# Kernel tuning notes

Hardware: AMD Instinct MI355X
Metric: run time of the kernel (lower is better)

The kernel has to match this reference:

```python
import math
import jax, jax.numpy as jnp
import numpy as np
from jax import lax

B, S, T = 16, 1200, 600
D, V, FF = 1024, 1404, 2048
H, DH, PERIOD, WID = 4, 256, 25, 8


def setup_inputs() -> dict:
    key = jax.random.key(0)
    ks = jax.random.split(key, 24)
    w = lambda i, shape: jax.random.normal(ks[i], shape, dtype=jnp.float32) * 0.02
    return {
        "audio_embedding": jax.random.normal(ks[0], (B, S, 768), dtype=jnp.float32),
        "vertice": jax.random.normal(ks[1], (B, T, 3, 468), dtype=jnp.float32),
        "W_af": w(2, (D, 768)), "b_af": w(3, (D,)),
        "sa_Wq": w(4, (D, D)), "sa_bq": w(5, (D,)),
        "sa_Wk": w(6, (D, D)), "sa_bk": w(7, (D,)),
        "sa_Wv": w(8, (D, D)), "sa_bv": w(9, (D,)),
        "sa_Wo": w(10, (D, D)), "sa_bo": w(11, (D,)),
        "ca_Wq": w(12, (D, D)), "ca_bq": w(13, (D,)),
        "ca_Wk": w(14, (D, D)), "ca_bk": w(15, (D,)),
        "ca_Wv": w(16, (D, D)), "ca_bv": w(17, (D,)),
        "ca_Wo": w(18, (D, D)), "ca_bo": w(19, (D,)),
        "ln1_g": jnp.ones((D,), jnp.float32), "ln1_b": jnp.zeros((D,), jnp.float32),
        "ln2_g": jnp.ones((D,), jnp.float32), "ln2_b": jnp.zeros((D,), jnp.float32),
        "ln3_g": jnp.ones((D,), jnp.float32), "ln3_b": jnp.zeros((D,), jnp.float32),
        "W_ff1": w(20, (FF, D)), "b_ff1": jnp.zeros((FF,), jnp.float32),
        "W_ff2": w(21, (D, FF)), "b_ff2": jnp.zeros((D,), jnp.float32),
        "W_vm": w(22, (D, V)), "b_vm": jnp.zeros((D,), jnp.float32),
        "W_vr": w(23, (V, D)), "b_vr": jnp.zeros((V,), jnp.float32),
    }


def _pe_table():
    # PeriodicPositionalEncoding: sin/cos table of length `period`, tiled over time
    pos = np.arange(PERIOD, dtype=np.float32)[:, None]
    div = np.exp(np.arange(0, D, 2, dtype=np.float32) * (-math.log(10000.0) / D))
    pe = np.zeros((PERIOD, D), dtype=np.float32)
    pe[:, 0::2] = np.sin(pos * div)
    pe[:, 1::2] = np.cos(pos * div)
    return jnp.asarray(pe)


def _slopes():
    start = 2.0 ** (-2.0 ** (-(math.log2(H) - 3.0)))
    return jnp.asarray(start * start ** np.arange(H, dtype=np.float32), dtype=jnp.float32)


def _ln(x, g, b):
    m = jnp.mean(x, -1, keepdims=True)
    v = jnp.mean((x - m) ** 2, -1, keepdims=True)
    return (x - m) / jnp.sqrt(v + 1e-5) * g + b


def reference(audio_embedding, vertice, W_af, b_af, sa_Wq, sa_bq, sa_Wk, sa_bk, sa_Wv, sa_bv, sa_Wo, sa_bo, ca_Wq, ca_bq, ca_Wk, ca_bk, ca_Wv, ca_bv, ca_Wo, ca_bo, ln1_g, ln1_b, ln2_g, ln2_b, ln3_g, ln3_b, W_ff1, b_ff1, W_ff2, b_ff2, W_vm, b_vm, W_vr, b_vr):
    # The torch loop reruns the full causal decoder on the growing prefix each frame;
    # because the tgt mask is strictly causal (ALiBi bias depends only on i-j), the
    # math is exactly equivalent to an incremental decode with a self-attn KV cache.
    pe, slopes = _pe_table(), _slopes()
    scale = 1.0 / math.sqrt(DH)
    NEG = -1e9
    hidden = audio_embedding @ W_af.T + b_af              # (B,S,D) audio_feature_map
    mem_k = (hidden @ ca_Wk.T + ca_bk).reshape(B, S, H, DH)
    mem_v = (hidden @ ca_Wv.T + ca_bv).reshape(B, S, H, DH)
    t_idx = jnp.arange(T)
    s_idx = jnp.arange(S)
    emb0 = jnp.broadcast_to(b_vm, (B, D))                 # vertice_map(zeros)
    kc0 = jnp.zeros((T, B, D), jnp.float32)
    vc0 = jnp.zeros((T, B, D), jnp.float32)

    def step(carry, i):
        emb, kc, vc = carry
        x = emb + pe[i % PERIOD]                          # PPE (B,D)
        q = (x @ sa_Wq.T + sa_bq).reshape(B, H, DH)
        kc = kc.at[i].set(x @ sa_Wk.T + sa_bk)
        vc = vc.at[i].set(x @ sa_Wv.T + sa_bv)
        kh = kc.reshape(T, B, H, DH)
        vh = vc.reshape(T, B, H, DH)
        rel = i - t_idx                                   # ALiBi: alibi[i,j] = -floor((i-j)/period)
        bias = slopes[:, None] * (-(jnp.maximum(rel, 0) // PERIOD)).astype(jnp.float32)
        sc = jnp.einsum('bhd,tbhd->bht', q, kh) * scale + bias[None]
        sc = jnp.where((t_idx <= i)[None, None, :], sc, NEG)
        sa = jnp.einsum('bht,tbhd->bhd', jax.nn.softmax(sc, -1), vh).reshape(B, D)
        x = _ln(x + sa @ sa_Wo.T + sa_bo, ln1_g, ln1_b)
        q2 = (x @ ca_Wq.T + ca_bq).reshape(B, H, DH)
        sc2 = jnp.einsum('bhd,bshd->bhs', q2, mem_k) * scale
        allowed = (s_idx >= 2 * i - (WID - 2)) & (s_idx < 2 * i + 2)   # enc_dec_mask window
        sc2 = jnp.where(allowed[None, None, :], sc2, NEG)
        ca = jnp.einsum('bhs,bshd->bhd', jax.nn.softmax(sc2, -1), mem_v).reshape(B, D)
        x = _ln(x + ca @ ca_Wo.T + ca_bo, ln2_g, ln2_b)
        ff = jax.nn.relu(x @ W_ff1.T + b_ff1) @ W_ff2.T + b_ff2
        x = _ln(x + ff, ln3_g, ln3_b)
        out_v = x @ W_vr.T + b_vr                         # vertice_map_r (B,V)
        emb_next = out_v @ W_vm.T + b_vm                  # vertice_map of last output
        return (emb_next, kc, vc), out_v

    _, outs = lax.scan(step, (emb0, kc0, vc0), t_idx)
    vertice_out = jnp.transpose(outs, (1, 0, 2))          # (B,T,V)
    loss = jnp.mean((vertice_out - vertice.reshape(B, T, -1)) ** 2)
    return loss
```

## Files before the change

### kernel.cpp

```cpp
#include <hip/hip_runtime.h>

typedef unsigned short u16;
typedef short s16x8 __attribute__((ext_vector_type(8)));
typedef float f32x4 __attribute__((ext_vector_type(4)));
typedef float f32x2 __attribute__((ext_vector_type(2)));
typedef unsigned u32x2 __attribute__((ext_vector_type(2)));

#define DEV static __device__ __forceinline__

DEV float bf2f(u16 h){ union{unsigned u;float f;} v; v.u=((unsigned)h)<<16; return v.f; }
DEV u16 f2bf(float f){ union{float f;unsigned u;} v; v.f=f; unsigned u=v.u; return (u16)((u + 0x7fffu + ((u>>16)&1u))>>16); }

DEV void st2_dc(u16* p, u16 v){
  unsigned vv = v;
  asm volatile("global_store_short %0, %1, off sc0 sc1" :: "v"(p), "v"(vv) : "memory");
}
DEV void st16_dc(void* p, s16x8 v){
  asm volatile("global_store_dwordx4 %0, %1, off sc0 sc1" :: "v"(p), "v"(v) : "memory");
}
DEV void stf_dc(float* p, float v){
  asm volatile("global_store_dword %0, %1, off sc0 sc1" :: "v"(p), "v"(v) : "memory");
}
DEV u16 ld2_dc(const u16* p){
  unsigned r;
  asm volatile("global_load_ushort %0, %1, off sc0 sc1\n\ts_waitcnt vmcnt(0)" : "=&v"(r) : "v"(p) : "memory");
  return (u16)r;
}
DEV u32x2 ld8_dc2(const u16* p){
  u32x2 r;
  asm volatile("global_load_dwordx2 %0, %1, off sc0 sc1\n\ts_waitcnt vmcnt(0)" : "=&v"(r) : "v"(p) : "memory");
  return r;
}
DEV void vmwait0(){ asm volatile("s_waitcnt vmcnt(0)" ::: "memory"); }

DEV void ldf8_dc(const u16* p, s16x8* o){
  asm volatile(
    "global_load_dwordx4 %0, %8, off sc0 sc1\n\t"
    "global_load_dwordx4 %1, %8, off offset:64 sc0 sc1\n\t"
    "global_load_dwordx4 %2, %8, off offset:128 sc0 sc1\n\t"
    "global_load_dwordx4 %3, %8, off offset:192 sc0 sc1\n\t"
    "global_load_dwordx4 %4, %8, off offset:256 sc0 sc1\n\t"
    "global_load_dwordx4 %5, %8, off offset:320 sc0 sc1\n\t"
    "global_load_dwordx4 %6, %8, off offset:384 sc0 sc1\n\t"
    "global_load_dwordx4 %7, %8, off offset:448 sc0 sc1\n\t"
    "s_waitcnt vmcnt(0)"
    : "=&v"(o[0]),"=&v"(o[1]),"=&v"(o[2]),"=&v"(o[3]),
      "=&v"(o[4]),"=&v"(o[5]),"=&v"(o[6]),"=&v"(o[7])
    : "v"(p) : "memory");
}
DEV void ldf8r_dc(const u16* p, s16x8* o, const u16* pr, unsigned* rr){
  asm volatile(
    "global_load_dwordx4 %0, %9, off sc0 sc1\n\t"
    "global_load_dwordx4 %1, %9, off offset:64 sc0 sc1\n\t"
    "global_load_dwordx4 %2, %9, off offset:128 sc0 sc1\n\t"
    "global_load_dwordx4 %3, %9, off offset:192 sc0 sc1\n\t"
    "global_load_dwordx4 %4, %9, off offset:256 sc0 sc1\n\t"
    "global_load_dwordx4 %5, %9, off offset:320 sc0 sc1\n\t"
    "global_load_dwordx4 %6, %9, off offset:384 sc0 sc1\n\t"
    "global_load_dwordx4 %7, %9, off offset:448 sc0 sc1\n\t"
    "global_load_ushort %8, %10, off sc0 sc1\n\t"
    "s_waitcnt vmcnt(0)"
    : "=&v"(o[0]),"=&v"(o[1]),"=&v"(o[2]),"=&v"(o[3]),
      "=&v"(o[4]),"=&v"(o[5]),"=&v"(o[6]),"=&v"(o[7]),"=&v"(*rr)
    : "v"(p), "v"(pr) : "memory");
}
DEV void ldf8rs_dc(const u16* p, s16x8* o, const u16* pr, unsigned* rr, const float* ps, f32x2* ss){
  asm volatile(
    "global_load_dwordx4 %0, %10, off sc0 sc1\n\t"
    "global_load_dwordx4 %1, %10, off offset:64 sc0 sc1\n\t"
    "global_load_dwordx4 %2, %10, off offset:128 sc0 sc1\n\t"
    "global_load_dwordx4 %3, %10, off offset:192 sc0 sc1\n\t"
    "global_load_dwordx4 %4, %10, off offset:256 sc0 sc1\n\t"
    "global_load_dwordx4 %5, %10, off offset:320 sc0 sc1\n\t"
    "global_load_dwordx4 %6, %10, off offset:384 sc0 sc1\n\t"
    "global_load_dwordx4 %7, %10, off offset:448 sc0 sc1\n\t"
    "global_load_ushort %8, %11, off sc0 sc1\n\t"
    "global_load_dwordx2 %9, %12, off sc0 sc1\n\t"
    "s_waitcnt vmcnt(0)"
    : "=&v"(o[0]),"=&v"(o[1]),"=&v"(o[2]),"=&v"(o[3]),
      "=&v"(o[4]),"=&v"(o[5]),"=&v"(o[6]),"=&v"(o[7]),"=&v"(*rr),"=&v"(*ss)
    : "v"(p), "v"(pr), "v"(ps) : "memory");
}
DEV void ldf16rs_dc(const u16* p, s16x8* o, const u16* pr, unsigned* rr, const float* ps, f32x2* ss){
  asm volatile(
    "global_load_dwordx4 %0, %18, off sc0 sc1\n\t"
    "global_load_dwordx4 %1, %18, off offset:64 sc0 sc1\n\t"
    "global_load_dwordx4 %2, %18, off offset:128 sc0 sc1\n\t"
    "global_load_dwordx4 %3, %18, off offset:192 sc0 sc1\n\t"
    "global_load_dwordx4 %4, %18, off offset:256 sc0 sc1\n\t"
    "global_load_dwordx4 %5, %18, off offset:320 sc0 sc1\n\t"
    "global_load_dwordx4 %6, %18, off offset:384 sc0 sc1\n\t"
    "global_load_dwordx4 %7, %18, off offset:448 sc0 sc1\n\t"
    "global_load_dwordx4 %8, %18, off offset:2048 sc0 sc1\n\t"
    "global_load_dwordx4 %9, %18, off offset:2112 sc0 sc1\n\t"
    "global_load_dwordx4 %10, %18, off offset:2176 sc0 sc1\n\t"
    "global_load_dwordx4 %11, %18, off offset:2240 sc0 sc1\n\t"
    "global_load_dwordx4 %12, %18, off offset:2304 sc0 sc1\n\t"
    "global_load_dwordx4 %13, %18, off offset:2368 sc0 sc1\n\t"
    "global_load_dwordx4 %14, %18, off offset:2432 sc0 sc1\n\t"
    "global_load_dwordx4 %15, %18, off offset:2496 sc0 sc1\n\t"
    "global_load_ushort %16, %19, off sc0 sc1\n\t"
    "global_load_dwordx2 %17, %20, off sc0 sc1\n\t"
    "s_waitcnt vmcnt(0)"
    : "=&v"(o[0]),"=&v"(o[1]),"=&v"(o[2]),"=&v"(o[3]),
      "=&v"(o[4]),"=&v"(o[5]),"=&v"(o[6]),"=&v"(o[7]),
      "=&v"(o[8]),"=&v"(o[9]),"=&v"(o[10]),"=&v"(o[11]),
      "=&v"(o[12]),"=&v"(o[13]),"=&v"(o[14]),"=&v"(o[15]),
      "=&v"(*rr),"=&v"(*ss)
    : "v"(p), "v"(pr), "v"(ps) : "memory");
}

constexpr size_t SZ_DD = (size_t)1024*1024*2;
constexpr size_t OFF_WQ2=0;
constexpr size_t OFF_WK2=OFF_WQ2+SZ_DD;
constexpr size_t OFF_WV2=OFF_WK2+SZ_DD;
constexpr size_t OFF_WO=OFF_WV2+SZ_DD;
constexpr size_t OFF_CAWQ=OFF_WO+SZ_DD;
constexpr size_t OFF_CAWO=OFF_CAWQ+SZ_DD;
constexpr size_t OFF_FF1=OFF_CAWO+SZ_DD;
constexpr size_t OFF_FF2=OFF_FF1+(size_t)2048*1024*2;
constexpr size_t OFF_MB =OFF_FF2+(size_t)2048*1024*2;
constexpr size_t OFF_WVR=OFF_MB+SZ_DD;
constexpr size_t OFF_WKP=OFF_WVR+(size_t)1404*1024*2;
constexpr size_t OFF_WVP=OFF_WKP+(size_t)1024*768*2;
constexpr size_t OFF_WAFT=OFF_WVP+(size_t)1024*768*2;
constexpr size_t OFF_WVRT=OFF_WAFT+(size_t)768*1024*2;
constexpr size_t OFF_PE  =OFF_WVRT+(size_t)1024*1408*2;
constexpr size_t OFF_BKP =OFF_PE+25*1024*4;
constexpr size_t OFF_BVP =OFF_BKP+4096;
constexpr size_t OFF_BCOMB=OFF_BVP+4096;
constexpr size_t OFF_MEMK=OFF_BCOMB+4096;
constexpr size_t OFF_MEMV=OFF_MEMK+(size_t)16*1200*1024*2;
constexpr size_t OFF_KC  =OFF_MEMV+(size_t)16*1200*1024*2;
constexpr size_t OFF_VC  =OFF_KC+(size_t)600*16*1024*2;
constexpr size_t OFF_U3S =OFF_VC+(size_t)600*16*1024*2;
constexpr size_t OFF_ST3 =OFF_U3S+(size_t)600*16*1024*2;
constexpr size_t OFF_XB  =OFF_ST3+600*32*4;
constexpr size_t OFF_QB  =OFF_XB+32768;
constexpr size_t OFF_SC  =OFF_QB+32768;
constexpr size_t OFF_SA  =OFF_SC+(size_t)16*4*608*4;
constexpr size_t OFF_U1  =OFF_SA+32768;
constexpr size_t OFF_ST1 =OFF_U1+32768;
constexpr size_t OFF_Q2  =OFF_ST1+256;
constexpr size_t OFF_CA  =OFF_Q2+32768;
constexpr size_t OFF_U2  =OFF_CA+32768;
constexpr size_t OFF_ST2 =OFF_U2+32768;
constexpr size_t OFF_HH  =OFF_ST2+256;
constexpr size_t OFF_LOSS=OFF_HH+65536;
constexpr size_t OFF_BAR =OFF_LOSS+256;
constexpr size_t OFF_MBT =OFF_BAR+32768;
constexpr size_t OFF_AT  =OFF_MBT+SZ_DD;
constexpr size_t WS_NEED =OFF_AT+(size_t)3*25*1024*4;

DEV float gemm_frag(const s16x8* a, const u16* slot, float* FB){
  int tid=threadIdx.x, wv=tid>>6, ln=tid&63;
  int r=ln&15, kq=ln>>4;
  int k0=wv*256 + kq*8;
  int sw=(r&7)<<3;
  const u16* bp = slot + r*1024;
  f32x4 acc={0.f,0.f,0.f,0.f};
  #pragma unroll
  for(int j=0;j<8;j++)
    acc = __builtin_amdgcn_mfma_f32_16x16x32_bf16(a[j], *(const s16x8*)(bp + ((k0+32*j)^sw)), acc, 0,0,0);
  #pragma unroll
  for(int j=0;j<4;j++) FB[wv*256 + (kq*4+j)*16 + r] = acc[j];
  __syncthreads();
  int row=tid>>4, col=tid&15;
  float s=(FB[row*16+col]+FB[256+row*16+col])+(FB[512+row*16+col]+FB[768+row*16+col]);
  __syncthreads();
  return s;
}

DEV void ln_frags(s16x8* a, const float* g, const float* be, int k0, int r, float* RB, float* STm, float* STr){
  int tid=threadIdx.x;
  float sum=0.f, sq=0.f;
  #pragma unroll
  for(int j=0;j<8;j++){
    #pragma unroll
    for(int e=0;e<8;e++){ float f=bf2f((u16)a[j][e]); sum+=f; sq+=f*f; }
  }
  RB[tid]=sum; RB[256+tid]=sq;
  __syncthreads();
  if (tid<16){
    float S=0.f,Q=0.f;
    #pragma unroll
    for(int q=0;q<16;q++){ S+=RB[tid+16*q]; Q+=RB[256+tid+16*q]; }
    float m=S*(1.f/1024.f); float var=Q*(1.f/1024.f)-m*m;
    STm[tid]=m; STr[tid]=rsqrtf(var+1e-5f);
  }
  __syncthreads();
  float m=STm[r], rs=STr[r];
  const float* gg=g+k0; const float* bb=be+k0;
  #pragma unroll
  for(int j=0;j<8;j++){
    s16x8 o;
    #pragma unroll
    for(int e=0;e<8;e++){ int k=32*j+e; float f=(bf2f((u16)a[j][e])-m)*rs*gg[k]+bb[k]; o[e]=(short)f2bf(f); }
    a[j]=o;
  }
}

DEV void copy_slot(const u16* src, int rstride, u16* dst){
  int row=threadIdx.x>>4, k0=(threadIdx.x&15)<<6;
  int sw=(row&7)<<3;
  const u16* s = src + (size_t)row*rstride + k0;
  u16* d = dst + row*1024;
  #pragma unroll
  for(int c=0;c<64;c+=8)
    *(s16x8*)(d + (((k0+c))^sw)) = *(const s16x8*)(s+c);
}

DEV void gbar(char* barb, unsigned& epoch, int wg){
  vmwait0();
  __syncthreads();
  unsigned target = epoch + 1u;
  if (threadIdx.x == 0)
    __hip_atomic_store((unsigned*)(barb + (wg<<7)), target, __ATOMIC_RELAXED, __HIP_MEMORY_SCOPE_AGENT);
  {
    unsigned* s = (unsigned*)(barb + (threadIdx.x<<7));
    while (__hip_atomic_load(s, __ATOMIC_RELAXED, __HIP_MEMORY_SCOPE_AGENT) < target)
      __builtin_amdgcn_s_sleep(1);
  }
  __syncthreads();
  epoch++;
}

__global__ void __launch_bounds__(256) k_init(float* pe, float* loss, unsigned* bar){
  int tid=threadIdx.x;
  if (tid==0) loss[0]=0.f;
  for(int idx=tid; idx<8192; idx+=256) bar[idx]=0u;
  for(int idx=tid; idx<25600; idx+=256){
    int p_=idx>>10, d_=idx&1023; int m=d_>>1;
    float div = expf(-(float)(2*m) * (9.210340372f/1024.f));
    float a = (float)p_ * div;
    pe[idx] = (d_&1)? cosf(a) : sinf(a);
  }
}

__global__ void __launch_bounds__(256) k_f2bf(const float* s, u16* d, int n){
  int idx=(blockIdx.x*256+threadIdx.x)*8;
  if (idx < n){
    #pragma unroll
    for(int j=0;j<8;j++) d[idx+j]=f2bf(s[idx+j]);
  }
}

__global__ void __launch_bounds__(256) k_tr(const float* src, int R, int C, u16* dst, int ldd){
  __shared__ float TL[32][33];
  int cb=(C+31)/32;
  int bj=blockIdx.x%cb, br=blockIdx.x/cb;
  int j0=bj*32, r0=br*32;
  int lj=threadIdx.x&31, lr=threadIdx.x>>5;
  #pragma unroll
  for(int p=0;p<4;p++){ int rr=r0+lr+p*8, jj=j0+lj;
    TL[lr+p*8][lj] = (rr<R && jj<C)? src[(size_t)rr*C+jj] : 0.f; }
  __syncthreads();
  #pragma unroll
  for(int p=0;p<4;p++){ int jj=j0+lr+p*8, rr=r0+lj;
    if (jj<C && rr<ldd) dst[(size_t)jj*ldd+rr] = f2bf(TL[lj][lr+p*8]); }
}

__global__ void __launch_bounds__(256) k_trb(const u16* src, u16* dst){
  __shared__ u16 T[32][33];
  int bi=blockIdx.x>>5, bj=blockIdx.x&31;
  int li=threadIdx.x>>5, lj=threadIdx.x&31;
  #pragma unroll
  for(int p=0;p<4;p++) T[li+p*8][lj] = src[(size_t)(bi*32+li+p*8)*1024 + bj*32+lj];
  __syncthreads();
  #pragma unroll
  for(int p=0;p<4;p++) dst[(size_t)(bj*32+li+p*8)*1024 + bi*32+lj] = T[lj][li+p*8];
}

DEV float gemm_tile16g(const u16* SLu, int lds_stride, const u16* W, int Kext, int wstride, int colbase, float* FB){
  int tid=threadIdx.x, wv=tid>>6, ln=tid&63;
  int r=ln&15, kq=ln>>4;
  int kpw=Kext>>2, k0=wv*kpw;
  const u16* ap = SLu + r*lds_stride + k0 + kq*8;
  const u16* bp = W + (size_t)(colbase+r)*wstride + k0 + kq*8;
  f32x4 acc={0.f,0.f,0.f,0.f};
  for(int k=0;k<kpw;k+=32)
    acc = __builtin_amdgcn_mfma_f32_16x16x32_bf16(*(const s16x8*)(ap+k), *(const s16x8*)(bp+k), acc, 0,0,0);
  #pragma unroll
  for(int j=0;j<4;j++) FB[wv*256 + (kq*4+j)*16 + r] = acc[j];
  __syncthreads();
  int row=tid>>4, col=tid&15;
  float s=(FB[row*16+col]+FB[256+row*16+col])+(FB[512+row*16+col]+FB[768+row*16+col]);
  __syncthreads();
  return s;
}

__global__ void __launch_bounds__(256) k_gemm_pre(const float* A, int lda, int Kreal, int Kpad,
                                                  const u16* Bw, u16* out, int ldo, int Ntiles){
  __shared__ u16 SL[16*1416];
  __shared__ float FB[1024];
  int bx=blockIdx.x; int mt=bx/Ntiles, nt=bx%Ntiles;
  int tid=threadIdx.x;
  int cpt = Kpad>>4;
  { int row=tid>>4, c0=(tid&15)*cpt;
    const float* s=A + (size_t)(mt*16+row)*lda;
    u16* d=SL + row*(Kpad+8);
    for(int c=0;c<cpt;c++){ int k=c0+c; d[k] = (k<Kreal)? f2bf(s[k]) : (u16)0; }
    __syncthreads();
  }
  float v = gemm_tile16g(SL, Kpad+8, Bw, Kpad, Kpad, nt*16, FB);
  int row=tid>>4, col=tid&15;
  out[(size_t)(mt*16+row)*ldo + nt*16+col] = f2bf(v);
}

__global__ void __launch_bounds__(256) k_bvec(const float* caWk, const float* ca_bk, const float* b_af,
                                              const float* caWv, const float* ca_bv,
                                              const float* Wvm, const float* b_vr, const float* b_vm,
                                              float* bkp, float* bvp, float* bcomb){
  __shared__ float VB[1408];
  int seg=blockIdx.x>>2, ch=blockIdx.x&3; int o=ch*256+threadIdx.x;
  const float* vec = (seg==2)? b_vr : b_af; int K = (seg==2)?1404:1024;
  for(int k=threadIdx.x;k<K;k+=256) VB[k]=vec[k];
  __syncthreads();
  const float* Arow = (seg==0)? caWk+(size_t)o*1024 : (seg==1)? caWv+(size_t)o*1024 : Wvm+(size_t)o*1404;
  float s=0.f;
  for(int k=0;k<K;k++) s += Arow[k]*VB[k];
  if(seg==0) bkp[o]=s+ca_bk[o]; else if(seg==1) bvp[o]=s+ca_bv[o]; else bcomb[o]=s+b_vm[o];
}

__global__ void __launch_bounds__(256) k_afold(const float* pe, const float* bcomb,
                                               const float* Wq, const float* Wk, const float* Wv,
                                               const float* bq, const float* bk, const float* bv,
                                               float* at){
  __shared__ float XV[1024];
  int bx=blockIdx.x; int mat=bx/100; int rem=bx%100; int ip=rem>>2; int ch=rem&3;
  const float* W = (mat==0)?Wq:(mat==1)?Wk:Wv;
  const float* bias = (mat==0)?bq:(mat==1)?bk:bv;
  for(int o=threadIdx.x;o<1024;o+=256) XV[o]=bcomb[o]+pe[ip*1024+o];
  __syncthreads();
  int c = ch*256+threadIdx.x;
  const float* wr = W + (size_t)c*1024;
  float acc=0.f;
  for(int o=0;o<1024;o++) acc += XV[o]*wr[o];
  at[((size_t)mat*25+ip)*1024+c] = acc + bias[c];
}

__global__ void __launch_bounds__(256) k_qkv0(const float* b_vm, const float* pe,
                                              const float* Wq, const float* Wk, const float* Wv,
                                              const float* bq, const float* bk, const float* bv,
                                              u16* qb, u16* kc, u16* vc, u16* xb){
  __shared__ float XV[1024];
  int bx=blockIdx.x; int mat=bx&3, ch=bx>>2;
  for(int o=threadIdx.x;o<1024;o+=256) XV[o]=b_vm[o]+pe[o];
  __syncthreads();
  int c = ch*256+threadIdx.x;
  if (mat==3){
    u16 hv = f2bf(XV[c]);
    for(int r=0;r<16;r++) xb[r*1024+c]=hv;
  } else {
    const float* W = (mat==0)?Wq:(mat==1)?Wk:Wv;
    const float* bias = (mat==0)?bq:(mat==1)?bk:bv;
    const float* wr = W + (size_t)c*1024;
    float acc=0.f;
    for(int o=0;o<1024;o++) acc += XV[o]*wr[o];
    u16 hv = f2bf(acc + bias[c]);
    u16* dst = (mat==0)? qb : (mat==1)? kc : vc;
    for(int r=0;r<16;r++) dst[r*1024+c]=hv;
  }
}

__global__ void __launch_bounds__(256) k_mem(const float* audio, const u16* wkp, const u16* wvp,
                                             const float* bkp, const float* bvp, u16* mt8, u16* memv){
  __shared__ u16 SL[16*776];
  int bx=blockIdx.x; int mt=bx>>3, cbk=bx&7;
  int tid=threadIdx.x, wv=tid>>6, ln=tid&63;
  { int row=tid>>4, c0=(tid&15)*48;
    const float* s = audio + (size_t)(mt*16+row)*768 + c0;
    u16* d = SL + row*776 + c0;
    #pragma unroll
    for(int c=0;c<48;c+=8){ s16x8 o;
      #pragma unroll
      for(int j=0;j<8;j++) o[j]=(short)f2bf(s[c+j]);
      *(s16x8*)(d+c)=o; }
    __syncthreads();
  }
  int r=ln&15, kq=ln>>4;
  const u16* ap = SL + r*776 + kq*8;
  for(int rep=0;rep<2;rep++){
    int colb = cbk*128 + wv*32 + rep*16;
    for(int mat=0;mat<2;mat++){
      const u16* W = mat? wvp : wkp;
      const u16* bp = W + (size_t)(colb+r)*768 + kq*8;
      f32x4 acc={0.f,0.f,0.f,0.f};
      for(int k=0;k<768;k+=32)
        acc = __builtin_amdgcn_mfma_f32_16x16x32_bf16(*(const s16x8*)(ap+k), *(const s16x8*)(bp+k), acc, 0,0,0);
      const float* bias = mat? bvp:bkp;
      int o = colb + r;
      float bo = bias[o];
      #pragma unroll
      for(int j=0;j<4;j++){ int row_=kq*4+j;
        int g = mt*16+row_;
        float val = acc[j] + bo;
        if (mat){
          memv[(size_t)g*1024 + o] = f2bf(val);
        } else {
          int bb=g/1200, ss=g-bb*1200;
          mt8[(((size_t)(bb*4 + (o>>8))*32 + ((o&255)>>3))*1200 + ss)*8 + (o&7)] = f2bf(val);
        }
      }
    }
  }
}

struct LoopArgs {
  const float *sa_bo,*ca_bq,*ca_bo,*b_ff1,*b_ff2;
  const float *g1,*be1,*g2,*be2,*g3,*be3;
  char* ws;
};

__global__ void __launch_bounds__(256,1) k_loop(LoopArgs A){
  __shared__ u16 WL[3*16*1024];
  __shared__ float FB[1024];
  __shared__ float PL[608];
  __shared__ float RB[640];
  __shared__ float STm[16], STr[16];

  char* ws = A.ws;
  const u16* wq2  =(const u16*)(ws+OFF_WQ2);
  const u16* wk2  =(const u16*)(ws+OFF_WK2);
  const u16* wv2  =(const u16*)(ws+OFF_WV2);
  const u16* wo   =(const u16*)(ws+OFF_WO);
  const u16* cawq =(const u16*)(ws+OFF_CAWQ);
  const u16* cawo =(const u16*)(ws+OFF_CAWO);
  const u16* ff1  =(const u16*)(ws+OFF_FF1);
  const u16* ff2  =(const u16*)(ws+OFF_FF2);
  const u16* mb   =(const u16*)(ws+OFF_MB);
  const float* pe =(const float*)(ws+OFF_PE);
  const float* bcomb=(const float*)(ws+OFF_BCOMB);
  const float* at =(const float*)(ws+OFF_AT);
  const u16* mt8  =(const u16*)(ws+OFF_MEMK);
  const u16* memv =(const u16*)(ws+OFF_MEMV);
  u16* kc =(u16*)(ws+OFF_KC);
  u16* vc =(u16*)(ws+OFF_VC);
  u16* u3s=(u16*)(ws+OFF_U3S);
  float* st3=(float*)(ws+OFF_ST3);
  u16* xb =(u16*)(ws+OFF_XB);
  u16* qb =(u16*)(ws+OFF_QB);
  u16* sab=(u16*)(ws+OFF_SA);
  u16* u1 =(u16*)(ws+OFF_U1);
  float* st1=(float*)(ws+OFF_ST1);
  u16* cab=(u16*)(ws+OFF_CA);
  u16* u2 =(u16*)(ws+OFF_U2);
  float* st2=(float*)(ws+OFF_ST2);
  u16* hh =(u16*)(ws+OFF_HH);
  char* barb=(char*)(ws+OFF_BAR);

  unsigned epoch = 0;
  int wg = blockIdx.x, tid = threadIdx.x;
  int row = tid>>4, lo = tid&15;
  int wv = tid>>6, ln = tid&63;
  int fr = ln&15, kq = ln>>4;
  int k0 = wv*256 + kq*8;
  int grp = wg>>6, ct = (wg&63)<<4;

  {
    u16* s0d = WL;          u16* s1d = WL+16384;  u16* s2d = WL+32768;
    if (grp==0){
      copy_slot(wq2 +(size_t)ct*1024,1024,s0d);
      copy_slot(ff1 +(size_t)ct*1024,1024,s2d);
    } else if (grp==1){
      copy_slot(wk2 +(size_t)ct*1024,1024,s0d);
      copy_slot(cawo+(size_t)ct*1024,1024,s1d);
      copy_slot(ff1 +((size_t)(1024+ct))*1024,1024,s2d);
    } else if (grp==2){
      copy_slot(wv2 +(size_t)ct*1024,1024,s0d);
      copy_slot(ff2 +(size_t)ct*2048,2048,s1d);
      copy_slot(ff2 +(size_t)ct*2048+1024,2048,s2d);
    } else {
      copy_slot(mb  +(size_t)ct*1024,1024,s0d);
      copy_slot(wo  +(size_t)ct*1024,1024,s1d);
    }
    __syncthreads();
  }
  const u16* SLOT0 = WL;
  const u16* SLOT1 = WL+16384;
  const u16* SLOT2 = WL+32768;

  #pragma unroll 1
  for (int i=0;i<600;i++){

    if (wg < 64){
      int b=wg>>2, h=wg&3, cnt=i+1;
      RB[tid] = bf2f(ld2_dc(qb + b*1024 + h*256 + tid));
      __syncthreads();
      float sl = 1.0f/(float)(4<<(2*h));
      float mloc=-1e30f, lloc=0.f;
      for(int t=tid; t<cnt; t+=256){
        const u16* kr = kc + ((size_t)t*16 + b)*1024 + h*256;
        float s=0.f;
        #pragma unroll
        for(int c=0;c<256;c+=8){
          s16x8 k8 = *(const s16x8*)(kr+c);
          #pragma unroll
          for(int j=0;j<8;j++) s += RB[c+j]*bf2f((u16)k8[j]);
        }
        s = s*0.0625f - sl*(float)((i-t)/25);
        PL[t]=s;
        float M = fmaxf(mloc, s);
        lloc = lloc*__expf(mloc-M) + __expf(s-M);
        mloc = M;
      }
      #pragma unroll
      for(int off=32; off>0; off>>=1){
        float m2=__shfl_xor(mloc,off), l2=__shfl_xor(lloc,off);
        float M=fmaxf(mloc,m2);
        lloc = lloc*__expf(mloc-M) + l2*__expf(m2-M);
        mloc = M;
      }
      if (ln==0){ RB[576+2*wv]=mloc; RB[577+2*wv]=lloc; }
      __syncthreads();
      float M=-1e30f, L=0.f;
      #pragma unroll
      for(int w=0;w<4;w++){
        float m2=RB[576+2*w], l2=RB[577+2*w];
        float Mn=fmaxf(M,m2);
        L = L*__expf(M-Mn) + l2*__expf(m2-Mn);
        M = Mn;
      }
      float rl = 1.0f/L;
      int d_oct = tid>>3, t_ln = tid&7;
      const u16* vcb = vc + (size_t)b*1024 + h*256 + d_oct*8;
      float acc[8]={0.f,0.f,0.f,0.f,0.f,0.f,0.f,0.f};
      for(int t=t_ln; t<cnt; t+=8){
        s16x8 v8 = *(const s16x8*)(vcb + (size_t)t*16384);
        float p = __expf(PL[t]-M);
        #pragma unroll
        for(int jj=0;jj<8;jj++) acc[jj] += p*bf2f((u16)v8[jj]);
      }
      #pragma unroll
      for(int j=0;j<8;j++){
        acc[j] += __shfl_xor(acc[j],1);
        acc[j] += __shfl_xor(acc[j],2);
        acc[j] += __shfl_xor(acc[j],4);
      }
      if (t_ln==0){
        s16x8 o8;
        #pragma unroll
        for(int j=0;j<8;j++) o8[j]=(short)f2bf(acc[j]*rl);
        st16_dc(sab + b*1024 + h*256 + d_oct*8, o8);
      }
    }
    gbar(barb, epoch, wg);

    if (wg>=192){
      s16x8 f[8]; unsigned er;
      ldf8r_dc(sab + fr*1024 + k0, f, xb + row*1024 + ct + lo, &er);
      float v = gemm_frag(f,SLOT1,FB);
      int o = ct+lo;
      st2_dc(u1 + row*1024 + o, f2bf(bf2f((u16)er) + v + A.sa_bo[o]));
    }
    gbar(barb, epoch, wg);

    if (wg<64){
      int b=wg>>2, h=wg&3;
      u32x2 uu = ld8_dc2(u1 + b*1024 + tid*4);
      float e0=bf2f((u16)(uu[0]&0xffffu)), e1=bf2f((u16)(uu[0]>>16));
      float e2=bf2f((u16)(uu[1]&0xffffu)), e3=bf2f((u16)(uu[1]>>16));
      float s=(e0+e1)+(e2+e3);
      float q=(e0*e0+e1*e1)+(e2*e2+e3*e3);
      #pragma unroll
      for(int o2=32;o2>0;o2>>=1){ s+=__shfl_down(s,o2); q+=__shfl_down(q,o2); }
      if (ln==0){ RB[608+wv]=s; RB[616+wv]=q; }
      __syncthreads();
      float S=(RB[608]+RB[609])+(RB[610]+RB[611]);
      float Q=(RB[616]+RB[617])+(RB[618]+RB[619]);
      float m=S*(1.f/1024.f);
      float rs=rsqrtf(Q*(1.f/1024.f)-m*m+1e-5f);
      if (h==0 && tid==0){ stf_dc(st1+b*2, m); stf_dc(st1+b*2+1, rs); }
      { int k=tid*4;
        FB[k]  =(e0-m)*rs*A.g1[k]  +A.be1[k];
        FB[k+1]=(e1-m)*rs*A.g1[k+1]+A.be1[k+1];
        FB[k+2]=(e2-m)*rs*A.g1[k+2]+A.be1[k+2];
        FB[k+3]=(e3-m)*rs*A.g1[k+3]+A.be1[k+3]; }
      __syncthreads();
      int c = h*256 + tid;
      const u16* wr = cawq + (size_t)c*1024;
      float acc=0.f;
      #pragma unroll 4
      for(int kk=0;kk<128;kk++){
        s16x8 w8 = *(const s16x8*)(wr + kk*8);
        #pragma unroll
        for(int j=0;j<8;j++) acc += FB[kk*8+j]*bf2f((u16)w8[j]);
      }
      RB[tid] = acc + A.ca_bq[c];
      __syncthreads();
      int s0 = 2*i-6; if(s0<0)s0=0;
      int s1 = 2*i+2; if(s1>1200)s1=1200;
      int ns = s1-s0;
      int si=tid>>5, dl=tid&31;
      float p=0.f;
      if (si<ns){
        const u16* MT = mt8 + (((size_t)(b*4+h)*32 + dl)*1200 + (s0+si))*8;
        s16x8 m8 = *(const s16x8*)MT;
        #pragma unroll
        for(int j=0;j<8;j++) p += RB[dl*8+j]*bf2f((u16)m8[j]);
      }
      #pragma unroll
      for(int o2=16;o2>0;o2>>=1) p += __shfl_xor(p,o2);
      if (dl==0 && si<ns) RB[512+si] = p*0.0625f;
      __syncthreads();
      float mx=-1e30f;
      for(int qd=0;qd<ns;qd++) mx=fmaxf(mx,RB[512+qd]);
      float l=0.f, acc2=0.f;
      for(int qd=0;qd<ns;qd++){
        float e=__expf(RB[512+qd]-mx); l+=e;
        acc2 += e*bf2f(memv[(size_t)(b*1200+s0+qd)*1024 + h*256 + tid]);
      }
      st2_dc(cab + b*1024+h*256+tid, f2bf(acc2/l));
    }
    gbar(barb, epoch, wg);

    if (wg>=64 && wg<128){
      s16x8 f[8]; unsigned ur; f32x2 sv;
      ldf8rs_dc(cab + fr*1024 + k0, f, u1 + row*1024 + ct + lo, &ur, st1 + row*2, &sv);
      float v = gemm_frag(f,SLOT1,FB);
      int o=ct+lo;
      float x1 = (bf2f((u16)ur)-sv[0])*sv[1]*A.g1[o] + A.be1[o];
      st2_dc(u2+row*1024+o, f2bf(x1 + v + A.ca_bo[o]));
    }
    gbar(barb, epoch, wg);

    if (wg<128){
      s16x8 f[8];
      ldf8_dc(u2 + fr*1024 + k0, f);
      ln_frags(f, A.g2, A.be2, k0, fr, RB, STm, STr);
      float v = gemm_frag(f,SLOT2,FB);
      int o=(wg<<4)+lo;
      st2_dc(hh+row*2048+o, f2bf(fmaxf(v + A.b_ff1[o], 0.f)));
      if (wg==0 && tid<16){ stf_dc(st2+tid*2,STm[tid]); stf_dc(st2+tid*2+1,STr[tid]); }
    }
    gbar(barb, epoch, wg);

    if (wg>=128 && wg<192){
      s16x8 f[16]; unsigned ur; f32x2 sv;
      ldf16rs_dc(hh + fr*2048 + k0, f, u2 + row*1024 + ct + lo, &ur, st2 + row*2, &sv);
      float v = gemm_frag(f,SLOT1,FB);
      v += gemm_frag(f+8,SLOT2,FB);
      int o=ct+lo;
      float x2 = (bf2f((u16)ur)-sv[0])*sv[1]*A.g2[o] + A.be2[o];
      st2_dc(u3s + ((size_t)i*16+row)*1024+o, f2bf(x2 + v + A.b_ff2[o]));
    }
    gbar(barb, epoch, wg);

    {
      int ipn = (i+1)%25;
      s16x8 f[8];
      ldf8_dc(u3s + (size_t)i*16384 + fr*1024 + k0, f);
      ln_frags(f, A.g3, A.be3, k0, fr, RB, STm, STr);
      float v = gemm_frag(f,SLOT0,FB);
      int o = ct+lo;
      if (grp==0){
        st2_dc(qb + row*1024 + o, f2bf(v + at[(size_t)0*25600 + ipn*1024 + o]));
      } else if (grp==1){
        if (i<599) st2_dc(kc + ((size_t)(i+1)*16+row)*1024 + o, f2bf(v + at[(size_t)1*25600 + ipn*1024 + o]));
      } else if (grp==2){
        if (i<599) st2_dc(vc + ((size_t)(i+1)*16+row)*1024 + o, f2bf(v + at[(size_t)2*25600 + ipn*1024 + o]));
      } else {
        st2_dc(xb + row*1024 + o, f2bf(v + bcomb[o] + pe[ipn*1024+o]));
        if (wg==192 && tid<16){ st3[i*32+tid*2]=STm[tid]; st3[i*32+tid*2+1]=STr[tid]; }
      }
    }
    gbar(barb, epoch, wg);
  }
}

__global__ void __launch_bounds__(256) k_loss(const u16* u3s, const float* st3, const u16* wvr,
                                              const float* bvr, const float* g3, const float* be3,
                                              const float* vert, float* loss){
  __shared__ u16 SL[16*1032];
  __shared__ float R[64];
  int bx=blockIdx.x; int ib=bx/11, cb=bx%11;
  int tid=threadIdx.x, wvv=tid>>6, ln=tid&63;
  int r=ln&15, kq=ln>>4;
  float lsum=0.f;
  for(int ii=0;ii<8;ii++){
    int i=ib*8+ii;
    { int row=tid>>4, c0=(tid&15)<<6;
      float m=st3[i*32+row*2], rs=st3[i*32+row*2+1];
      const u16* s=u3s + (size_t)(i*16+row)*1024 + c0;
      u16* d=SL + row*1032 + c0;
      #pragma unroll
      for(int c=0;c<64;c+=8){ s16x8 v=*(const s16x8*)(s+c); s16x8 o;
        #pragma unroll
        for(int j=0;j<8;j++){ int cc=c0+c+j; o[j]=(short)f2bf((bf2f((u16)v[j])-m)*rs*g3[cc]+be3[cc]); }
        *(s16x8*)(d+c)=o; }
      __syncthreads();
    }
    const u16* ap = SL + r*1032 + kq*8;
    for(int rep=0;rep<2;rep++){
      int colb = cb*128 + wvv*32 + rep*16;
      int o_r = colb + r; bool ok = o_r < 1404;
      const u16* bp = wvr + (size_t)(ok? o_r:0)*1024 + kq*8;
      f32x4 acc={0.f,0.f,0.f,0.f};
      for(int k=0;k<1024;k+=32)
        acc = __builtin_amdgcn_mfma_f32_16x16x32_bf16(*(const s16x8*)(ap+k), *(const s16x8*)(bp+k), acc, 0,0,0);
      if (ok){
        float bo = bvr[o_r];
        #pragma unroll
        for(int j=0;j<4;j++){
          int b_=kq*4+j;
          float ov = acc[j] + bo;
          float vt = vert[(size_t)(b_*600 + i)*1404 + o_r];
          float dd = ov - vt; lsum += dd*dd;
        }
      }
    }
    __syncthreads();
  }
  #pragma unroll
  for(int o=32;o>0;o>>=1) lsum += __shfl_down(lsum,o);
  if (ln==0) R[wvv]=lsum;
  __syncthreads();
  if (tid==0) atomicAdd(loss, (R[0]+R[1])+(R[2]+R[3]));
}

__global__ void k_fin(const float* loss, float* dout){
  if (threadIdx.x==0) dout[0] = loss[0] * (1.f/13478400.f);
}

extern "C" void kernel_launch(void* const* d_in, const int* in_sizes, int n_in,
                              void* d_out, int out_size, void* d_ws, size_t ws_size,
                              hipStream_t stream){
  char* ws = (char*)d_ws;
  if (ws_size < WS_NEED){ hipMemsetAsync(d_out, 0, 4, stream); return; }

  const float* audio=(const float*)d_in[0];
  const float* vert =(const float*)d_in[1];
  const float* W_af =(const float*)d_in[2];
  const float* b_af =(const float*)d_in[3];
  const float* saWq =(const float*)d_in[4];  const float* sa_bq=(const float*)d_in[5];
  const float* saWk =(const float*)d_in[6];  const float* sa_bk=(const float*)d_in[7];
  const float* saWv =(const float*)d_in[8];  const float* sa_bv=(const float*)d_in[9];
  const float* saWo =(const float*)d_in[10]; const float* sa_bo=(const float*)d_in[11];
  const float* caWq =(const float*)d_in[12]; const float* ca_bq=(const float*)d_in[13];
  const float* caWk =(const float*)d_in[14]; const float* ca_bk=(const float*)d_in[15];
  const float* caWv =(const float*)d_in[16]; const float* ca_bv=(const float*)d_in[17];
  const float* caWo =(const float*)d_in[18]; const float* ca_bo=(const float*)d_in[19];
  const float* g1=(const float*)d_in[20]; const float* be1=(const float*)d_in[21];
  const float* g2=(const float*)d_in[22]; const float* be2=(const float*)d_in[23];
  const float* g3=(const float*)d_in[24]; const float* be3=(const float*)d_in[25];
  const float* Wff1=(const float*)d_in[26]; const float* b_ff1=(const float*)d_in[27];
  const float* Wff2=(const float*)d_in[28]; const float* b_ff2=(const float*)d_in[29];
  const float* Wvm=(const float*)d_in[30];  const float* b_vm=(const float*)d_in[31];
  const float* Wvr=(const float*)d_in[32];  const float* b_vr=(const float*)d_in[33];

  k_init<<<1,256,0,stream>>>((float*)(ws+OFF_PE), (float*)(ws+OFF_LOSS), (unsigned*)(ws+OFF_BAR));

  k_f2bf<<<512,256,0,stream>>>(caWq,(u16*)(ws+OFF_CAWQ),1048576);
  k_f2bf<<<512,256,0,stream>>>(caWo,(u16*)(ws+OFF_CAWO),1048576);
  k_f2bf<<<512,256,0,stream>>>(saWo,(u16*)(ws+OFF_WO),1048576);
  k_f2bf<<<1024,256,0,stream>>>(Wff1,(u16*)(ws+OFF_FF1),2097152);
  k_f2bf<<<1024,256,0,stream>>>(Wff2,(u16*)(ws+OFF_FF2),2097152);
  k_f2bf<<<702,256,0,stream>>>(Wvr,(u16*)(ws+OFF_WVR),1437696);

  k_tr<<<24*32,256,0,stream>>>(W_af, 1024, 768, (u16*)(ws+OFF_WAFT), 1024);
  k_tr<<<32*44,256,0,stream>>>(Wvr, 1404, 1024, (u16*)(ws+OFF_WVRT), 1408);

  k_gemm_pre<<<64*48,256,0,stream>>>(caWk, 1024, 1024, 1024, (const u16*)(ws+OFF_WAFT), (u16*)(ws+OFF_WKP), 768, 48);
  k_gemm_pre<<<64*48,256,0,stream>>>(caWv, 1024, 1024, 1024, (const u16*)(ws+OFF_WAFT), (u16*)(ws+OFF_WVP), 768, 48);
  k_gemm_pre<<<64*64,256,0,stream>>>(Wvm, 1404, 1404, 1408, (const u16*)(ws+OFF_WVRT), (u16*)(ws+OFF_MB), 1024, 64);

  k_trb<<<1024,256,0,stream>>>((const u16*)(ws+OFF_MB), (u16*)(ws+OFF_MBT));
  k_gemm_pre<<<64*64,256,0,stream>>>(saWq, 1024, 1024, 1024, (const u16*)(ws+OFF_MBT), (u16*)(ws+OFF_WQ2), 1024, 64);
  k_gemm_pre<<<64*64,256,0,stream>>>(saWk, 1024, 1024, 1024, (const u16*)(ws+OFF_MBT), (u16*)(ws+OFF_WK2), 1024, 64);
  k_gemm_pre<<<64*64,256,0,stream>>>(saWv, 1024, 1024, 1024, (const u16*)(ws+OFF_MBT), (u16*)(ws+OFF_WV2), 1024, 64);

  k_bvec<<<12,256,0,stream>>>(caWk, ca_bk, b_af, caWv, ca_bv, Wvm, b_vr, b_vm,
                              (float*)(ws+OFF_BKP),(float*)(ws+OFF_BVP),(float*)(ws+OFF_BCOMB));

  k_afold<<<300,256,0,stream>>>((const float*)(ws+OFF_PE), (const float*)(ws+OFF_BCOMB),
                                saWq, saWk, saWv, sa_bq, sa_bk, sa_bv, (float*)(ws+OFF_AT));

  k_qkv0<<<16,256,0,stream>>>(b_vm, (const float*)(ws+OFF_PE), saWq, saWk, saWv, sa_bq, sa_bk, sa_bv,
                              (u16*)(ws+OFF_QB), (u16*)(ws+OFF_KC), (u16*)(ws+OFF_VC), (u16*)(ws+OFF_XB));

  k_mem<<<9600,256,0,stream>>>(audio, (const u16*)(ws+OFF_WKP),(const u16*)(ws+OFF_WVP),
                               (const float*)(ws+OFF_BKP),(const float*)(ws+OFF_BVP),
                               (u16*)(ws+OFF_MEMK),(u16*)(ws+OFF_MEMV));

  LoopArgs la{ sa_bo, ca_bq, ca_bo, b_ff1, b_ff2,
               g1, be1, g2, be2, g3, be3, ws };
  k_loop<<<256,256,0,stream>>>(la);

  k_loss<<<825,256,0,stream>>>((const u16*)(ws+OFF_U3S),(const float*)(ws+OFF_ST3),
                               (const u16*)(ws+OFF_WVR), b_vr, g3, be3, vert, (float*)(ws+OFF_LOSS));
  k_fin<<<1,64,0,stream>>>((const float*)(ws+OFF_LOSS), (float*)d_out);
}
```

Baseline: 41.64 ms.

## Compute cross-attention query projection with LDS-resident weights across 64 workgroups

```diff
diff --git a/kernel.cpp b/kernel.cpp
--- a/kernel.cpp
+++ b/kernel.cpp
@@ -25,11 +25,6 @@
   unsigned r;
   asm volatile("global_load_ushort %0, %1, off sc0 sc1\n\ts_waitcnt vmcnt(0)" : "=&v"(r) : "v"(p) : "memory");
   return (u16)r;
-}
-DEV u32x2 ld8_dc2(const u16* p){
-  u32x2 r;
-  asm volatile("global_load_dwordx2 %0, %1, off sc0 sc1\n\ts_waitcnt vmcnt(0)" : "=&v"(r) : "v"(p) : "memory");
-  return r;
 }
 DEV void vmwait0(){ asm volatile("s_waitcnt vmcnt(0)" ::: "memory"); }
 
@@ -443,6 +438,7 @@
   u16* sab=(u16*)(ws+OFF_SA);
   u16* u1 =(u16*)(ws+OFF_U1);
   float* st1=(float*)(ws+OFF_ST1);
+  u16* q2b=(u16*)(ws+OFF_Q2);
   u16* cab=(u16*)(ws+OFF_CA);
   u16* u2 =(u16*)(ws+OFF_U2);
   float* st2=(float*)(ws+OFF_ST2);
@@ -461,6 +457,7 @@
     u16* s0d = WL;          u16* s1d = WL+16384;  u16* s2d = WL+32768;
     if (grp==0){
       copy_slot(wq2 +(size_t)ct*1024,1024,s0d);
+      copy_slot(cawq+(size_t)ct*1024,1024,s1d);
       copy_slot(ff1 +(size_t)ct*1024,1024,s2d);
     } else if (grp==1){
       copy_slot(wk2 +(size_t)ct*1024,1024,s0d);
@@ -556,37 +553,19 @@
     gbar(barb, epoch, wg);
 
     if (wg<64){
+      s16x8 f[8];
+      ldf8_dc(u1 + fr*1024 + k0, f);
+      ln_frags(f, A.g1, A.be1, k0, fr, RB, STm, STr);
+      float v = gemm_frag(f,SLOT1,FB);
+      int o=ct+lo;
+      st2_dc(q2b + row*1024+o, f2bf(v + A.ca_bq[o]));
+      if (wg==0 && tid<16){ stf_dc(st1+tid*2, STm[tid]); stf_dc(st1+tid*2+1, STr[tid]); }
+    }
+    gbar(barb, epoch, wg);
+
+    if (wg<64){
       int b=wg>>2, h=wg&3;
-      u32x2 uu = ld8_dc2(u1 + b*1024 + tid*4);
-      float e0=bf2f((u16)(uu[0]&0xffffu)), e1=bf2f((u16)(uu[0]>>16));
-      float e2=bf2f((u16)(uu[1]&0xffffu)), e3=bf2f((u16)(uu[1]>>16));
-      float s=(e0+e1)+(e2+e3);
-      float q=(e0*e0+e1*e1)+(e2*e2+e3*e3);
-      #pragma unroll
-      for(int o2=32;o2>0;o2>>=1){ s+=__shfl_down(s,o2); q+=__shfl_down(q,o2); }
-      if (ln==0){ RB[608+wv]=s; RB[616+wv]=q; }
-      __syncthreads();
-      float S=(RB[608]+RB[609])+(RB[610]+RB[611]);
-      float Q=(RB[616]+RB[617])+(RB[618]+RB[619]);
-      float m=S*(1.f/1024.f);
-      float rs=rsqrtf(Q*(1.f/1024.f)-m*m+1e-5f);
-      if (h==0 && tid==0){ stf_dc(st1+b*2, m); stf_dc(st1+b*2+1, rs); }
-      { int k=tid*4;
-        FB[k]  =(e0-m)*rs*A.g1[k]  +A.be1[k];
-        FB[k+1]=(e1-m)*rs*A.g1[k+1]+A.be1[k+1];
-        FB[k+2]=(e2-m)*rs*A.g1[k+2]+A.be1[k+2];
-        FB[k+3]=(e3-m)*rs*A.g1[k+3]+A.be1[k+3]; }
-      __syncthreads();
-      int c = h*256 + tid;
-      const u16* wr = cawq + (size_t)c*1024;
-      float acc=0.f;
-      #pragma unroll 4
-      for(int kk=0;kk<128;kk++){
-        s16x8 w8 = *(const s16x8*)(wr + kk*8);
-        #pragma unroll
-        for(int j=0;j<8;j++) acc += FB[kk*8+j]*bf2f((u16)w8[j]);
-      }
-      RB[tid] = acc + A.ca_bq[c];
+      RB[tid] = bf2f(ld2_dc(q2b + b*1024 + h*256 + tid));
       __syncthreads();
       int s0 = 2*i-6; if(s0<0)s0=0;
       int s1 = 2*i+2; if(s1>1200)s1=1200;
```

Result: faster. 34.44 ms (-17.3%).
